# Performance work log

Measured on AMD Instinct MI355X. Metric: run time of the kernel, lower is better.

The kernel has to match this reference:

```python
import jax, jax.numpy as jnp
import numpy as np

EPS = 1e-06

def rmsnorm(x, w):
    x32 = x.astype(jnp.float32)
    var = jnp.mean(x32 * x32, axis=-1, keepdims=True)
    return w * (x32 * jax.lax.rsqrt(var + EPS)).astype(x.dtype)

def setup_inputs() -> dict:
    B, T, C = 16, 256, 16
    token_dim, text_dim = 1024, 512
    key = jax.random.key(0)
    ks = jax.random.split(key, 8)
    token_embeds = jax.random.normal(ks[0], (B, T, token_dim), dtype=jnp.float32)
    char_embeds = jax.random.normal(ks[1], (B, T, C, text_dim), dtype=jnp.float32)
    filler_embed = jax.random.normal(ks[2], (text_dim,), dtype=jnp.float32)
    mask = jax.random.randint(ks[3], (B, T, C), 0, 2).astype(bool)
    mask = mask.at[0].set(True)  # force max valid count == T*C (static output shape)
    token_ids_mask = jnp.ones((B, T), dtype=bool)
    # xavier-uniform-ish weights
    def xav(k, fan_out, fan_in, gain=1.0):
        lim = gain * np.sqrt(6.0 / (fan_in + fan_out))
        return jax.random.uniform(k, (fan_out, fan_in), jnp.float32, -lim, lim)
    W_down = xav(ks[4], text_dim, token_dim)
    W_proj = xav(ks[5], 3, text_dim, gain=0.2)
    W_fusion = xav(ks[6], text_dim, text_dim)
    w_pre = jnp.ones((token_dim,), jnp.float32)
    w_tok = jnp.ones((text_dim,), jnp.float32)
    w_char = jnp.ones((text_dim,), jnp.float32)
    return {"token_embeds": token_embeds, "token_ids_mask": token_ids_mask,
            "char_embeds": char_embeds, "char_ids_mask": mask,
            "filler_embed": filler_embed, "w_pre": w_pre, "w_tok": w_tok,
            "w_char": w_char, "W_down": W_down, "W_proj": W_proj,
            "W_fusion": W_fusion, "max_valid_chars": T * C}

def reference(token_embeds, token_ids_mask, char_embeds, char_ids_mask,
              filler_embed, w_pre, w_tok, w_char, W_down, W_proj, W_fusion,
              max_valid_chars):
    B, T, C, d = char_embeds.shape
    MV = int(max_valid_chars)
    tok = rmsnorm(token_embeds, w_pre)                       # [B,T,token_dim]
    feats = rmsnorm(jnp.einsum('btk,dk->btd', tok, W_down), w_tok)  # [B,T,d]
    params = jnp.einsum('btd,pd->btp', jax.nn.silu(feats), W_proj)  # [B,T,3]
    scale = params[..., 0][:, :, None, None]                 # [B,T,1,1]
    shift = params[..., 1][:, :, None, None]
    gate = jax.nn.sigmoid(params[..., 2][:, :, None, None])
    cn = rmsnorm(char_embeds, w_char)                        # [B,T,C,d]
    fused = jnp.einsum('btcd,ed->btce', jax.nn.silu(cn * (1.0 + scale) + shift), W_fusion)
    fused = gate * fused + (1.0 - gate) * cn                 # [B,T,C,d]
    flat = fused.reshape(B, T * C, d)
    m = char_ids_mask.reshape(B, T * C).astype(jnp.int32)
    pos = jnp.cumsum(m, axis=1) - 1                          # dest within row
    offs = jnp.arange(B, dtype=jnp.int32)[:, None] * MV
    idx = jnp.where(m > 0, offs + pos, B * MV)               # invalid -> dump slot
    buf = jnp.broadcast_to(filler_embed, (B * MV + 1, d))
    buf = buf.at[idx.reshape(-1)].set(flat.reshape(-1, d))
    return buf[: B * MV].reshape(B, MV, d)
```

## Files before the change

### kernel.cpp

```cpp
#include <hip/hip_runtime.h>
#include <cstdint>
#include <cstddef>

#define EPS 1e-6f

typedef short bf16x8 __attribute__((ext_vector_type(8)));
typedef float f32x4  __attribute__((ext_vector_type(4)));

__device__ __forceinline__ short f2bf(float x) {
    uint32_t u = __builtin_bit_cast(uint32_t, x);
    return (short)((u + 0x7FFFu + ((u >> 16) & 1u)) >> 16);
}

__global__ __launch_bounds__(1024) void k_scan(const void* __restrict__ maskp,
                                               int* __restrict__ v_list,
                                               int* __restrict__ counts) {
    __shared__ int wtot[16];
    __shared__ int woff[16];
    __shared__ int mode_s;
    const int tid = threadIdx.x, lane = tid & 63, wave = tid >> 6;
    const int b = blockIdx.x;

    if (tid == 0) mode_s = 0;
    __syncthreads();
    {
        const int bad = (((const uint32_t*)maskp)[tid & 1023] > 1u) ? 1 : 0;
        if (bad) mode_s = 1;
    }
    __syncthreads();
    const int byte_mode = mode_s;

    int f0, f1, f2, f3;
    if (byte_mode) {
        const uint32_t v = ((const uint32_t*)maskp)[(b << 10) + tid];
        f0 = (v & 0x000000ffu) != 0;
        f1 = (v & 0x0000ff00u) != 0;
        f2 = (v & 0x00ff0000u) != 0;
        f3 = (v & 0xff000000u) != 0;
    } else {
        const uint4 v = ((const uint4*)maskp)[(b << 10) + tid];
        f0 = v.x != 0; f1 = v.y != 0; f2 = v.z != 0; f3 = v.w != 0;
    }
    const int c = f0 + f1 + f2 + f3;

    int incl = c;
#pragma unroll
    for (int off = 1; off < 64; off <<= 1) {
        const int n = __shfl_up(incl, off);
        if (lane >= off) incl += n;
    }
    if (lane == 63) wtot[wave] = incl;
    __syncthreads();
    if (tid == 0) {
        int run = 0;
#pragma unroll
        for (int wv = 0; wv < 16; ++wv) { woff[wv] = run; run += wtot[wv]; }
        counts[b] = run;
    }
    __syncthreads();

    int base = woff[wave] + incl - c;
    const int i0 = tid * 4;
    int* vl = v_list + (b << 12);
    if (f0) vl[base++] = i0;
    if (f1) vl[base++] = i0 + 1;
    if (f2) vl[base++] = i0 + 2;
    if (f3) vl[base++] = i0 + 3;
}

__global__ __launch_bounds__(256) void k_conv2(const float* __restrict__ srcA,
                                               short* __restrict__ dstA, int n4a,
                                               const float* __restrict__ srcB,
                                               short* __restrict__ dstB, int n4b) {
    const int gid = blockIdx.x * 256 + threadIdx.x;
    const float* s;
    short* d;
    int i;
    if (gid < n4a) { s = srcA; d = dstA; i = gid; }
    else {
        i = gid - n4a;
        if (i >= n4b) return;
        s = srcB; d = dstB;
    }
    const float4 v = ((const float4*)s)[i];
    short4 o;
    o.x = f2bf(v.x); o.y = f2bf(v.y); o.z = f2bf(v.z); o.w = f2bf(v.w);
    ((short4*)d)[i] = o;
}

__global__ __launch_bounds__(256) void k_tokprep(const float* __restrict__ tokens,
                                                 const float* __restrict__ w_pre,
                                                 short* __restrict__ tokbf) {
    const int tid = threadIdx.x, lane = tid & 63, wave = tid >> 6;
    const int row = blockIdx.x * 4 + wave;
    const float* xp = tokens + (size_t)row * 1024 + lane * 16;
    float4 x[4];
#pragma unroll
    for (int q = 0; q < 4; ++q) x[q] = *(const float4*)&xp[q * 4];
    float ss = 0.f;
#pragma unroll
    for (int q = 0; q < 4; ++q)
        ss += x[q].x * x[q].x + x[q].y * x[q].y + x[q].z * x[q].z + x[q].w * x[q].w;
#pragma unroll
    for (int off = 32; off > 0; off >>= 1) ss += __shfl_down(ss, off);
    ss = __shfl(ss, 0);
    const float r = rsqrtf(ss * (1.0f / 1024.0f) + EPS);
    const float* wp = w_pre + lane * 16;
    short* op = tokbf + (size_t)row * 1024 + lane * 16;
#pragma unroll
    for (int h = 0; h < 2; ++h) {
        bf16x8 o;
#pragma unroll
        for (int q = 0; q < 2; ++q) {
            const float4 wv = *(const float4*)&wp[h * 8 + q * 4];
            const float4 xv = x[h * 2 + q];
            o[q * 4 + 0] = f2bf(xv.x * wv.x * r);
            o[q * 4 + 1] = f2bf(xv.y * wv.y * r);
            o[q * 4 + 2] = f2bf(xv.z * wv.z * r);
            o[q * 4 + 3] = f2bf(xv.w * wv.w * r);
        }
        *(bf16x8*)&op[h * 8] = o;
    }
}

__global__ __launch_bounds__(256) void k_gemm_tok(const short* __restrict__ tokbf,
                                                  const short* __restrict__ Wdbf,
                                                  float* __restrict__ feats) {
    __shared__ short As[128 * 32];
    __shared__ short Bs[128 * 32];
    const int tid = threadIdx.x, lane = tid & 63, w = tid >> 6;
    const int kt = blockIdx.x >> 7;
    const int mt = (blockIdx.x >> 2) & 31, nt = blockIdx.x & 3;
    const int wm = w >> 1, wn = w & 1;
    const int kbase = kt * 512;
    const short* hA = tokbf + (size_t)mt * 128 * 1024;
    const short* wB = Wdbf + (size_t)nt * 128 * 1024;

    f32x4 acc[4][4];
#pragma unroll
    for (int mi = 0; mi < 4; ++mi)
#pragma unroll
        for (int ni = 0; ni < 4; ++ni) acc[mi][ni] = (f32x4)0.f;

    const int rA = lane & 15, q8 = (lane >> 4) * 8;
    for (int kk = 0; kk < 512; kk += 32) {
#pragma unroll
        for (int q = 0; q < 2; ++q) {
            const int cid = (w * 2 + q) * 64 + lane;
            const int r = cid >> 2, kc = cid & 3;
            const size_t go = (size_t)r * 1024 + kbase + kk + kc * 8;
            __builtin_amdgcn_global_load_lds(
                (const __attribute__((address_space(1))) uint32_t*)(hA + go),
                (__attribute__((address_space(3))) uint32_t*)&As[(w * 2 + q) * 512], 16, 0, 0);
            __builtin_amdgcn_global_load_lds(
                (const __attribute__((address_space(1))) uint32_t*)(wB + go),
                (__attribute__((address_space(3))) uint32_t*)&Bs[(w * 2 + q) * 512], 16, 0, 0);
        }
        __syncthreads();
        bf16x8 af[4], bfr[4];
#pragma unroll
        for (int mi = 0; mi < 4; ++mi)
            af[mi] = *(const bf16x8*)&As[(wm * 64 + mi * 16 + rA) * 32 + q8];
#pragma unroll
        for (int ni = 0; ni < 4; ++ni)
            bfr[ni] = *(const bf16x8*)&Bs[(wn * 64 + ni * 16 + rA) * 32 + q8];
#pragma unroll
        for (int mi = 0; mi < 4; ++mi)
#pragma unroll
            for (int ni = 0; ni < 4; ++ni)
                acc[mi][ni] = __builtin_amdgcn_mfma_f32_16x16x32_bf16(af[mi], bfr[ni], acc[mi][ni], 0, 0, 0);
        __syncthreads();
    }
    float* fo = feats + (size_t)kt * 4096 * 512;
    const int rowb = mt * 128 + wm * 64 + (lane >> 4) * 4;
    const int colb = nt * 128 + wn * 64 + (lane & 15);
#pragma unroll
    for (int mi = 0; mi < 4; ++mi)
#pragma unroll
        for (int ni = 0; ni < 4; ++ni)
#pragma unroll
            for (int rg = 0; rg < 4; ++rg)
                fo[(size_t)(rowb + mi * 16 + rg) * 512 + colb + ni * 16] = acc[mi][ni][rg];
}

__global__ __launch_bounds__(64) void k_params(
    const float* __restrict__ feats_pre, const float* __restrict__ w_tok,
    const float* __restrict__ W_proj, float* __restrict__ params) {
    const int tk = blockIdx.x;
    const int lane = threadIdx.x;
    const int d0 = lane * 8;
    const float* fp0 = feats_pre + (size_t)tk * 512 + d0;
    const float* fp1 = fp0 + (size_t)4096 * 512;
    const float4 a0 = *(const float4*)&fp0[0];
    const float4 a1 = *(const float4*)&fp0[4];
    const float4 b0 = *(const float4*)&fp1[0];
    const float4 b1 = *(const float4*)&fp1[4];
    const float4 f0 = make_float4(a0.x + b0.x, a0.y + b0.y, a0.z + b0.z, a0.w + b0.w);
    const float4 f1 = make_float4(a1.x + b1.x, a1.y + b1.y, a1.z + b1.z, a1.w + b1.w);
    float ss = f0.x * f0.x + f0.y * f0.y + f0.z * f0.z + f0.w * f0.w
             + f1.x * f1.x + f1.y * f1.y + f1.z * f1.z + f1.w * f1.w;
#pragma unroll
    for (int off = 32; off > 0; off >>= 1) ss += __shfl_down(ss, off);
    ss = __shfl(ss, 0);
    const float rms = rsqrtf(ss * (1.0f / 512.0f) + EPS);

    const float4 wt0 = *(const float4*)&w_tok[d0];
    const float4 wt1 = *(const float4*)&w_tok[d0 + 4];
    float fv[8] = {f0.x, f0.y, f0.z, f0.w, f1.x, f1.y, f1.z, f1.w};
    float wv[8] = {wt0.x, wt0.y, wt0.z, wt0.w, wt1.x, wt1.y, wt1.z, wt1.w};
    float s[8];
#pragma unroll
    for (int j = 0; j < 8; ++j) {
        const float v = fv[j] * wv[j] * rms;
        s[j] = v / (1.0f + expf(-v));
    }
    float p[3];
#pragma unroll
    for (int q = 0; q < 3; ++q) {
        const float* Wp = W_proj + (size_t)q * 512 + d0;
        const float4 a = *(const float4*)&Wp[0];
        const float4 c = *(const float4*)&Wp[4];
        p[q] = s[0] * a.x + s[1] * a.y + s[2] * a.z + s[3] * a.w
             + s[4] * c.x + s[5] * c.y + s[6] * c.z + s[7] * c.w;
#pragma unroll
        for (int off = 32; off > 0; off >>= 1) p[q] += __shfl_down(p[q], off);
    }
    if (lane == 0) {
        float* po = params + (size_t)tk * 4;
        po[0] = 1.0f + p[0];
        po[1] = p[1];
        po[2] = 1.0f / (1.0f + expf(-p[2]));
    }
}

__global__ __launch_bounds__(256) void k_prep(
    const float* __restrict__ chars, const float* __restrict__ w_char,
    const float* __restrict__ params, const int* __restrict__ v_list,
    const int* __restrict__ counts, short* __restrict__ hb,
    float* __restrict__ rms_l, float* __restrict__ g_l) {
    const int tid = threadIdx.x, lane = tid & 63, wave = tid >> 6;
    const int b = blockIdx.x >> 10;
    const int j = (blockIdx.x & 1023) * 4 + wave;
    const int cnt = counts[b];
    const int cpad = (cnt + 127) & ~127;
    if (j >= cpad) return;
    short* hrow = hb + ((size_t)(b << 12) + j) * 512 + lane * 8;
    if (j >= cnt) {
        *(bf16x8*)hrow = (bf16x8)0;
        return;
    }
    const int i = v_list[(b << 12) + j];
    const float* xp = chars + ((size_t)(b << 12) + i) * 512 + lane * 8;
    const float4 x0 = *(const float4*)&xp[0];
    const float4 x1 = *(const float4*)&xp[4];
    float ss = x0.x * x0.x + x0.y * x0.y + x0.z * x0.z + x0.w * x0.w
             + x1.x * x1.x + x1.y * x1.y + x1.z * x1.z + x1.w * x1.w;
#pragma unroll
    for (int off = 32; off > 0; off >>= 1) ss += __shfl_down(ss, off);
    ss = __shfl(ss, 0);
    const float rms = rsqrtf(ss * (1.0f / 512.0f) + EPS);
    const float* pp = params + (size_t)((b << 8) + (i >> 4)) * 4;
    const float s1 = pp[0], sh = pp[1], g = pp[2];
    const float4 w0 = *(const float4*)&w_char[lane * 8];
    const float4 w1 = *(const float4*)&w_char[lane * 8 + 4];
    float xv[8] = {x0.x, x0.y, x0.z, x0.w, x1.x, x1.y, x1.z, x1.w};
    float wv[8] = {w0.x, w0.y, w0.z, w0.w, w1.x, w1.y, w1.z, w1.w};
    bf16x8 o;
#pragma unroll
    for (int q = 0; q < 8; ++q) {
        const float cn = wv[q] * xv[q] * rms;
        const float a = cn * s1 + sh;
        o[q] = f2bf(a / (1.0f + expf(-a)));
    }
    *(bf16x8*)hrow = o;
    if (lane == 0) {
        rms_l[(b << 12) + j] = rms;
        g_l[(b << 12) + j] = g;
    }
}

__global__ __launch_bounds__(256) void k_gemm_fus(
    const short* __restrict__ hb, const short* __restrict__ Wbf,
    const float* __restrict__ chars, const float* __restrict__ w_char,
    const float* __restrict__ rms_l, const float* __restrict__ g_l,
    const int* __restrict__ v_list, const int* __restrict__ counts,
    const float* __restrict__ filler, float* __restrict__ out) {
    __shared__ short As[128 * 32];
    __shared__ short Bs[128 * 32];
    __shared__ float g_s[128], rms_s[128];
    __shared__ int idx_s[128];
    const int tid = threadIdx.x, lane = tid & 63, w = tid >> 6;
    const int b = blockIdx.x >> 7;
    const int mt = (blockIdx.x >> 2) & 31;
    const int nt = blockIdx.x & 3;
    const int cnt = counts[b];
    const int row0 = mt * 128;
    if (row0 >= cnt) {
        const int colb = nt * 128;
        const float4 f = ((const float4*)(filler + colb))[tid & 31];
        float* o0 = out + ((size_t)(b << 12) + row0) * 512 + colb + (tid & 31) * 4;
#pragma unroll
        for (int r = (tid >> 5); r < 128; r += 8)
            *(float4*)&o0[(size_t)r * 512] = f;
        return;
    }
    const int wm = w >> 1, wn = w & 1;

    if (tid < 128) {
        const int j = row0 + tid;
        const bool valid = j < cnt;
        idx_s[tid] = valid ? v_list[(b << 12) + j] : 0;
        g_s[tid]   = valid ? g_l[(b << 12) + j] : 0.f;
        rms_s[tid] = valid ? rms_l[(b << 12) + j] : 0.f;
    }

    const short* hA = hb + ((size_t)(b << 12) + row0) * 512;
    const short* wB = Wbf + (size_t)nt * 128 * 512;

    f32x4 acc[4][4];
#pragma unroll
    for (int mi = 0; mi < 4; ++mi)
#pragma unroll
        for (int ni = 0; ni < 4; ++ni) acc[mi][ni] = (f32x4)0.f;

    const int rA = lane & 15, q8 = (lane >> 4) * 8;
    for (int kk = 0; kk < 512; kk += 32) {
#pragma unroll
        for (int q = 0; q < 2; ++q) {
            const int cid = (w * 2 + q) * 64 + lane;
            const int r = cid >> 2, kc = cid & 3;
            const size_t go = (size_t)r * 512 + kk + kc * 8;
            __builtin_amdgcn_global_load_lds(
                (const __attribute__((address_space(1))) uint32_t*)(hA + go),
                (__attribute__((address_space(3))) uint32_t*)&As[(w * 2 + q) * 512], 16, 0, 0);
            __builtin_amdgcn_global_load_lds(
                (const __attribute__((address_space(1))) uint32_t*)(wB + go),
                (__attribute__((address_space(3))) uint32_t*)&Bs[(w * 2 + q) * 512], 16, 0, 0);
        }
        __syncthreads();
        bf16x8 af[4], bfr[4];
#pragma unroll
        for (int mi = 0; mi < 4; ++mi)
            af[mi] = *(const bf16x8*)&As[(wm * 64 + mi * 16 + rA) * 32 + q8];
#pragma unroll
        for (int ni = 0; ni < 4; ++ni)
            bfr[ni] = *(const bf16x8*)&Bs[(wn * 64 + ni * 16 + rA) * 32 + q8];
#pragma unroll
        for (int mi = 0; mi < 4; ++mi)
#pragma unroll
            for (int ni = 0; ni < 4; ++ni)
                acc[mi][ni] = __builtin_amdgcn_mfma_f32_16x16x32_bf16(af[mi], bfr[ni], acc[mi][ni], 0, 0, 0);
        __syncthreads();
    }

    const int colb = nt * 128 + wn * 64 + (lane & 15);
    float wcv[4];
#pragma unroll
    for (int ni = 0; ni < 4; ++ni) wcv[ni] = w_char[colb + ni * 16];
#pragma unroll
    for (int mi = 0; mi < 4; ++mi) {
#pragma unroll
        for (int rg = 0; rg < 4; ++rg) {
            const int jl = wm * 64 + mi * 16 + (lane >> 4) * 4 + rg;
            const int j = row0 + jl;
            const size_t orow = ((size_t)(b << 12) + j) * 512;
            if (j < cnt) {
                const float g = g_s[jl], rm = rms_s[jl];
                const size_t xrow = ((size_t)(b << 12) + idx_s[jl]) * 512;
#pragma unroll
                for (int ni = 0; ni < 4; ++ni) {
                    const int col = colb + ni * 16;
                    const float x = chars[xrow + col];
                    const float cn = wcv[ni] * x * rm;
                    out[orow + col] = g * acc[mi][ni][rg] + (1.0f - g) * cn;
                }
            } else {
#pragma unroll
                for (int ni = 0; ni < 4; ++ni) {
                    const int col = colb + ni * 16;
                    out[orow + col] = filler[col];
                }
            }
        }
    }
}

extern "C" void kernel_launch(void* const* d_in, const int* in_sizes, int n_in,
                              void* d_out, int out_size, void* d_ws, size_t ws_size,
                              hipStream_t stream) {
    const float* tokens = (const float*)d_in[0];
    const float* chars  = (const float*)d_in[2];
    const void*  cmask  = d_in[3];
    const float* filler = (const float*)d_in[4];
    const float* w_pre  = (const float*)d_in[5];
    const float* w_tok  = (const float*)d_in[6];
    const float* w_char = (const float*)d_in[7];
    const float* W_down = (const float*)d_in[8];
    const float* W_proj = (const float*)d_in[9];
    const float* W_fus  = (const float*)d_in[10];
    float* out = (float*)d_out;

    float* feats_pre = (float*)d_ws;
    float* params    = feats_pre + (size_t)2 * 4096 * 512;
    int*   counts    = (int*)(params + (size_t)4096 * 4);
    int*   v_list    = counts + 16;
    float* rms_l     = (float*)(v_list + 65536);
    float* g_l       = rms_l + 65536;
    short* Wbf       = (short*)(g_l + 65536);
    short* hb        = Wbf + (size_t)512 * 512;
    short* tokbf     = hb + (size_t)16 * 4096 * 512;
    short* Wdbf      = tokbf + (size_t)4096 * 1024;

    k_scan<<<16, 1024, 0, stream>>>(cmask, v_list, counts);
    k_conv2<<<768, 256, 0, stream>>>(W_fus, Wbf, 65536, W_down, Wdbf, 131072);
    k_tokprep<<<1024, 256, 0, stream>>>(tokens, w_pre, tokbf);
    k_gemm_tok<<<256, 256, 0, stream>>>(tokbf, Wdbf, feats_pre);
    k_params<<<4096, 64, 0, stream>>>(feats_pre, w_tok, W_proj, params);
    k_prep<<<16384, 256, 0, stream>>>(chars, w_char, params, v_list, counts, hb, rms_l, g_l);
    k_gemm_fus<<<2048, 256, 0, stream>>>(hb, Wbf, chars, w_char, rms_l, g_l, v_list, counts, filler, out);
}
```

Before: 339.8 us.

## Fuse char prep into fusion GEMM and merge front kernels into one launch

Removes the separate k_prep kernel. The fusion GEMM now gathers char rows directly, computes the RMS per row, applies the scale/shift SiLU and converts to bf16 on the fly into swizzled LDS, which avoids writing and re-reading the bf16 activation buffer. The scan, weight conversion and token-prep kernels are merged into one launch, and the output stores become nontemporal with a remapped block order. The trade is that each of the four N-tiles per row block recomputes the RMS and the SiLU, and global_load_lds async copies are replaced by register-staged loads.

```diff
diff --git a/kernel.cpp b/kernel.cpp
--- a/kernel.cpp
+++ b/kernel.cpp
@@ -12,114 +12,111 @@
     return (short)((u + 0x7FFFu + ((u >> 16) & 1u)) >> 16);
 }
 
-__global__ __launch_bounds__(1024) void k_scan(const void* __restrict__ maskp,
-                                               int* __restrict__ v_list,
-                                               int* __restrict__ counts) {
-    __shared__ int wtot[16];
-    __shared__ int woff[16];
-    __shared__ int mode_s;
-    const int tid = threadIdx.x, lane = tid & 63, wave = tid >> 6;
-    const int b = blockIdx.x;
-
-    if (tid == 0) mode_s = 0;
-    __syncthreads();
-    {
-        const int bad = (((const uint32_t*)maskp)[tid & 1023] > 1u) ? 1 : 0;
-        if (bad) mode_s = 1;
-    }
-    __syncthreads();
-    const int byte_mode = mode_s;
-
-    int f0, f1, f2, f3;
-    if (byte_mode) {
-        const uint32_t v = ((const uint32_t*)maskp)[(b << 10) + tid];
-        f0 = (v & 0x000000ffu) != 0;
-        f1 = (v & 0x0000ff00u) != 0;
-        f2 = (v & 0x00ff0000u) != 0;
-        f3 = (v & 0xff000000u) != 0;
+__global__ __launch_bounds__(256) void k_front(
+    const void* __restrict__ maskp, int* __restrict__ v_list, int* __restrict__ counts,
+    const float* __restrict__ Wf, short* __restrict__ Wfbf,
+    const float* __restrict__ Wd, short* __restrict__ Wdbf,
+    const float* __restrict__ tokens, const float* __restrict__ w_pre,
+    short* __restrict__ tokbf) {
+    const int blk = blockIdx.x, tid = threadIdx.x;
+    if (blk < 16) {
+        __shared__ int wtot[4], woff[4];
+        __shared__ int mode_s;
+        const int b = blk, lane = tid & 63, wave = tid >> 6;
+        if (tid == 0) mode_s = 0;
+        __syncthreads();
+        {
+            int bad = 0;
+#pragma unroll
+            for (int q = 0; q < 4; ++q)
+                bad |= (((const uint32_t*)maskp)[q * 256 + tid] > 1u) ? 1 : 0;
+            if (bad) mode_s = 1;
+        }
+        __syncthreads();
+        int f[16];
+        if (mode_s) {
+            const uint4 v = ((const uint4*)maskp)[(b << 8) + tid];
+            const uint32_t ws[4] = {v.x, v.y, v.z, v.w};
+#pragma unroll
+            for (int q = 0; q < 4; ++q) {
+                f[q * 4 + 0] = (ws[q] & 0x000000ffu) != 0;
+                f[q * 4 + 1] = (ws[q] & 0x0000ff00u) != 0;
+                f[q * 4 + 2] = (ws[q] & 0x00ff0000u) != 0;
+                f[q * 4 + 3] = (ws[q] & 0xff000000u) != 0;
+            }
+        } else {
+            const uint4* mp = (const uint4*)maskp + ((size_t)b << 10) + tid * 4;
+#pragma unroll
+            for (int q = 0; q < 4; ++q) {
+                const uint4 v = mp[q];
+                f[q * 4 + 0] = v.x != 0; f[q * 4 + 1] = v.y != 0;
+                f[q * 4 + 2] = v.z != 0; f[q * 4 + 3] = v.w != 0;
+            }
+        }
+        int c = 0;
+#pragma unroll
+        for (int q = 0; q < 16; ++q) c += f[q];
+        int incl = c;
+#pragma unroll
+        for (int off = 1; off < 64; off <<= 1) {
+            const int n = __shfl_up(incl, off);
+            if (lane >= off) incl += n;
+        }
+        if (lane == 63) wtot[wave] = incl;
+        __syncthreads();
+        if (tid == 0) {
+            int run = 0;
+#pragma unroll
+            for (int wv = 0; wv < 4; ++wv) { woff[wv] = run; run += wtot[wv]; }
+            counts[b] = run;
+        }
+        __syncthreads();
+        int base = woff[wave] + incl - c;
+        int* vl = v_list + (b << 12);
+        const int i0 = tid * 16;
+#pragma unroll
+        for (int q = 0; q < 16; ++q)
+            if (f[q]) vl[base++] = i0 + q;
+    } else if (blk < 784) {
+        const int gid = (blk - 16) * 256 + tid;
+        const float* s; short* d; int i;
+        if (gid < 65536) { s = Wf; d = Wfbf; i = gid; }
+        else             { s = Wd; d = Wdbf; i = gid - 65536; }
+        const float4 v = ((const float4*)s)[i];
+        short4 o;
+        o.x = f2bf(v.x); o.y = f2bf(v.y); o.z = f2bf(v.z); o.w = f2bf(v.w);
+        ((short4*)d)[i] = o;
     } else {
-        const uint4 v = ((const uint4*)maskp)[(b << 10) + tid];
-        f0 = v.x != 0; f1 = v.y != 0; f2 = v.z != 0; f3 = v.w != 0;
-    }
-    const int c = f0 + f1 + f2 + f3;
-
-    int incl = c;
-#pragma unroll
-    for (int off = 1; off < 64; off <<= 1) {
-        const int n = __shfl_up(incl, off);
-        if (lane >= off) incl += n;
-    }
-    if (lane == 63) wtot[wave] = incl;
-    __syncthreads();
-    if (tid == 0) {
-        int run = 0;
-#pragma unroll
-        for (int wv = 0; wv < 16; ++wv) { woff[wv] = run; run += wtot[wv]; }
-        counts[b] = run;
-    }
-    __syncthreads();
-
-    int base = woff[wave] + incl - c;
-    const int i0 = tid * 4;
-    int* vl = v_list + (b << 12);
-    if (f0) vl[base++] = i0;
-    if (f1) vl[base++] = i0 + 1;
-    if (f2) vl[base++] = i0 + 2;
-    if (f3) vl[base++] = i0 + 3;
-}
-
-__global__ __launch_bounds__(256) void k_conv2(const float* __restrict__ srcA,
-                                               short* __restrict__ dstA, int n4a,
-                                               const float* __restrict__ srcB,
-                                               short* __restrict__ dstB, int n4b) {
-    const int gid = blockIdx.x * 256 + threadIdx.x;
-    const float* s;
-    short* d;
-    int i;
-    if (gid < n4a) { s = srcA; d = dstA; i = gid; }
-    else {
-        i = gid - n4a;
-        if (i >= n4b) return;
-        s = srcB; d = dstB;
-    }
-    const float4 v = ((const float4*)s)[i];
-    short4 o;
-    o.x = f2bf(v.x); o.y = f2bf(v.y); o.z = f2bf(v.z); o.w = f2bf(v.w);
-    ((short4*)d)[i] = o;
-}
-
-__global__ __launch_bounds__(256) void k_tokprep(const float* __restrict__ tokens,
-                                                 const float* __restrict__ w_pre,
-                                                 short* __restrict__ tokbf) {
-    const int tid = threadIdx.x, lane = tid & 63, wave = tid >> 6;
-    const int row = blockIdx.x * 4 + wave;
-    const float* xp = tokens + (size_t)row * 1024 + lane * 16;
-    float4 x[4];
-#pragma unroll
-    for (int q = 0; q < 4; ++q) x[q] = *(const float4*)&xp[q * 4];
-    float ss = 0.f;
-#pragma unroll
-    for (int q = 0; q < 4; ++q)
-        ss += x[q].x * x[q].x + x[q].y * x[q].y + x[q].z * x[q].z + x[q].w * x[q].w;
-#pragma unroll
-    for (int off = 32; off > 0; off >>= 1) ss += __shfl_down(ss, off);
-    ss = __shfl(ss, 0);
-    const float r = rsqrtf(ss * (1.0f / 1024.0f) + EPS);
-    const float* wp = w_pre + lane * 16;
-    short* op = tokbf + (size_t)row * 1024 + lane * 16;
-#pragma unroll
-    for (int h = 0; h < 2; ++h) {
-        bf16x8 o;
-#pragma unroll
-        for (int q = 0; q < 2; ++q) {
-            const float4 wv = *(const float4*)&wp[h * 8 + q * 4];
-            const float4 xv = x[h * 2 + q];
-            o[q * 4 + 0] = f2bf(xv.x * wv.x * r);
-            o[q * 4 + 1] = f2bf(xv.y * wv.y * r);
-            o[q * 4 + 2] = f2bf(xv.z * wv.z * r);
-            o[q * 4 + 3] = f2bf(xv.w * wv.w * r);
-        }
-        *(bf16x8*)&op[h * 8] = o;
+        const int lane = tid & 63, wave = tid >> 6;
+        const int row = (blk - 784) * 4 + wave;
+        const float* xp = tokens + (size_t)row * 1024 + lane * 16;
+        float4 x[4];
+#pragma unroll
+        for (int q = 0; q < 4; ++q) x[q] = *(const float4*)&xp[q * 4];
+        float ss = 0.f;
+#pragma unroll
+        for (int q = 0; q < 4; ++q)
+            ss += x[q].x * x[q].x + x[q].y * x[q].y + x[q].z * x[q].z + x[q].w * x[q].w;
+#pragma unroll
+        for (int off = 32; off > 0; off >>= 1) ss += __shfl_down(ss, off);
+        ss = __shfl(ss, 0);
+        const float r = rsqrtf(ss * (1.0f / 1024.0f) + EPS);
+        const float* wp = w_pre + lane * 16;
+        short* op = tokbf + (size_t)row * 1024 + lane * 16;
+#pragma unroll
+        for (int h = 0; h < 2; ++h) {
+            bf16x8 o;
+#pragma unroll
+            for (int q = 0; q < 2; ++q) {
+                const float4 wv = *(const float4*)&wp[h * 8 + q * 4];
+                const float4 xv = x[h * 2 + q];
+                o[q * 4 + 0] = f2bf(xv.x * wv.x * r);
+                o[q * 4 + 1] = f2bf(xv.y * wv.y * r);
+                o[q * 4 + 2] = f2bf(xv.z * wv.z * r);
+                o[q * 4 + 3] = f2bf(xv.w * wv.w * r);
+            }
+            *(bf16x8*)&op[h * 8] = o;
+        }
     }
 }
 
@@ -230,121 +227,136 @@
         po[0] = 1.0f + p[0];
         po[1] = p[1];
         po[2] = 1.0f / (1.0f + expf(-p[2]));
-    }
-}
-
-__global__ __launch_bounds__(256) void k_prep(
-    const float* __restrict__ chars, const float* __restrict__ w_char,
-    const float* __restrict__ params, const int* __restrict__ v_list,
-    const int* __restrict__ counts, short* __restrict__ hb,
-    float* __restrict__ rms_l, float* __restrict__ g_l) {
-    const int tid = threadIdx.x, lane = tid & 63, wave = tid >> 6;
-    const int b = blockIdx.x >> 10;
-    const int j = (blockIdx.x & 1023) * 4 + wave;
-    const int cnt = counts[b];
-    const int cpad = (cnt + 127) & ~127;
-    if (j >= cpad) return;
-    short* hrow = hb + ((size_t)(b << 12) + j) * 512 + lane * 8;
-    if (j >= cnt) {
-        *(bf16x8*)hrow = (bf16x8)0;
-        return;
-    }
-    const int i = v_list[(b << 12) + j];
-    const float* xp = chars + ((size_t)(b << 12) + i) * 512 + lane * 8;
-    const float4 x0 = *(const float4*)&xp[0];
-    const float4 x1 = *(const float4*)&xp[4];
-    float ss = x0.x * x0.x + x0.y * x0.y + x0.z * x0.z + x0.w * x0.w
-             + x1.x * x1.x + x1.y * x1.y + x1.z * x1.z + x1.w * x1.w;
-#pragma unroll
-    for (int off = 32; off > 0; off >>= 1) ss += __shfl_down(ss, off);
-    ss = __shfl(ss, 0);
-    const float rms = rsqrtf(ss * (1.0f / 512.0f) + EPS);
-    const float* pp = params + (size_t)((b << 8) + (i >> 4)) * 4;
-    const float s1 = pp[0], sh = pp[1], g = pp[2];
-    const float4 w0 = *(const float4*)&w_char[lane * 8];
-    const float4 w1 = *(const float4*)&w_char[lane * 8 + 4];
-    float xv[8] = {x0.x, x0.y, x0.z, x0.w, x1.x, x1.y, x1.z, x1.w};
-    float wv[8] = {w0.x, w0.y, w0.z, w0.w, w1.x, w1.y, w1.z, w1.w};
-    bf16x8 o;
-#pragma unroll
-    for (int q = 0; q < 8; ++q) {
-        const float cn = wv[q] * xv[q] * rms;
-        const float a = cn * s1 + sh;
-        o[q] = f2bf(a / (1.0f + expf(-a)));
-    }
-    *(bf16x8*)hrow = o;
-    if (lane == 0) {
-        rms_l[(b << 12) + j] = rms;
-        g_l[(b << 12) + j] = g;
+        po[3] = 0.f;
     }
 }
 
 __global__ __launch_bounds__(256) void k_gemm_fus(
-    const short* __restrict__ hb, const short* __restrict__ Wbf,
-    const float* __restrict__ chars, const float* __restrict__ w_char,
-    const float* __restrict__ rms_l, const float* __restrict__ g_l,
+    const short* __restrict__ Wbf, const float* __restrict__ chars,
+    const float* __restrict__ w_char, const float* __restrict__ params,
     const int* __restrict__ v_list, const int* __restrict__ counts,
     const float* __restrict__ filler, float* __restrict__ out) {
-    __shared__ short As[128 * 32];
-    __shared__ short Bs[128 * 32];
-    __shared__ float g_s[128], rms_s[128];
-    __shared__ int idx_s[128];
+    const int wg = (blockIdx.x & 7) * 256 + (blockIdx.x >> 3);
+    const int b = wg >> 7;
+    const int mt = (wg >> 2) & 31;
+    const int nt = wg & 3;
     const int tid = threadIdx.x, lane = tid & 63, w = tid >> 6;
-    const int b = blockIdx.x >> 7;
-    const int mt = (blockIdx.x >> 2) & 31;
-    const int nt = blockIdx.x & 3;
     const int cnt = counts[b];
     const int row0 = mt * 128;
     if (row0 >= cnt) {
-        const int colb = nt * 128;
-        const float4 f = ((const float4*)(filler + colb))[tid & 31];
-        float* o0 = out + ((size_t)(b << 12) + row0) * 512 + colb + (tid & 31) * 4;
-#pragma unroll
-        for (int r = (tid >> 5); r < 128; r += 8)
-            *(float4*)&o0[(size_t)r * 512] = f;
+        const int colb0 = nt * 128;
+        const f32x4 f = *(const f32x4*)(filler + colb0 + (tid & 31) * 4);
+        float* o0 = out + ((size_t)(b << 12) + row0) * 512 + colb0 + (tid & 31) * 4;
+        for (int r = tid >> 5; r < 128; r += 8)
+            __builtin_nontemporal_store(f, (f32x4*)&o0[(size_t)r * 512]);
         return;
     }
-    const int wm = w >> 1, wn = w & 1;
+
+    __shared__ short As[128 * 32];
+    __shared__ short Bs[128 * 32];
+    __shared__ float wc_s[512];
+    __shared__ float rmsv[128], s1v[128], shv[128], gv[128];
+    __shared__ int idxv[128];
+
+    wc_s[tid] = w_char[tid];
+    wc_s[tid + 256] = w_char[tid + 256];
 
     if (tid < 128) {
         const int j = row0 + tid;
         const bool valid = j < cnt;
-        idx_s[tid] = valid ? v_list[(b << 12) + j] : 0;
-        g_s[tid]   = valid ? g_l[(b << 12) + j] : 0.f;
-        rms_s[tid] = valid ? rms_l[(b << 12) + j] : 0.f;
-    }
-
-    const short* hA = hb + ((size_t)(b << 12) + row0) * 512;
-    const short* wB = Wbf + (size_t)nt * 128 * 512;
-
+        const int idx = valid ? v_list[(b << 12) + j] : -1;
+        idxv[tid] = idx;
+        if (valid) {
+            const float* pp = params + (size_t)((b << 8) + (idx >> 4)) * 4;
+            s1v[tid] = pp[0]; shv[tid] = pp[1]; gv[tid] = pp[2];
+        } else {
+            s1v[tid] = 0.f; shv[tid] = 0.f; gv[tid] = 0.f;
+        }
+    }
+    __syncthreads();
+
+    {
+        const int g16 = tid >> 4, l16 = tid & 15;
+#pragma unroll
+        for (int rr = 0; rr < 8; ++rr) {
+            const int r = g16 * 8 + rr;
+            const int id = idxv[r];
+            float ss = 0.f;
+            if (id >= 0) {
+                const float* rp = chars + (((size_t)(b << 12) + id) << 9) + l16 * 4;
+#pragma unroll
+                for (int s = 0; s < 8; ++s) {
+                    const float4 v = *(const float4*)&rp[s * 64];
+                    ss += v.x * v.x + v.y * v.y + v.z * v.z + v.w * v.w;
+                }
+            }
+#pragma unroll
+            for (int off = 8; off > 0; off >>= 1) ss += __shfl_down(ss, off);
+            if (l16 == 0) rmsv[r] = rsqrtf(ss * (1.0f / 512.0f) + EPS);
+        }
+    }
+    __syncthreads();
+
+    const int wm = w >> 1, wn = w & 1;
     f32x4 acc[4][4];
 #pragma unroll
     for (int mi = 0; mi < 4; ++mi)
 #pragma unroll
         for (int ni = 0; ni < 4; ++ni) acc[mi][ni] = (f32x4)0.f;
 
-    const int rA = lane & 15, q8 = (lane >> 4) * 8;
+    const int r2 = tid >> 1, hf = tid & 1;
+    const int swzA = ((r2 >> 1) & 3) << 3;
+    const float rmsr = rmsv[r2], s1r = s1v[r2], shr = shv[r2];
+    const int idr = idxv[r2];
+    const float* arow = (idr >= 0) ? (chars + (((size_t)(b << 12) + idr) << 9)) : nullptr;
+    const short* brow = Wbf + ((size_t)(nt * 128 + r2) << 9) + hf * 16;
+
+    const int rA = lane & 15;
+    const int ch = lane >> 4;
+
     for (int kk = 0; kk < 512; kk += 32) {
-#pragma unroll
-        for (int q = 0; q < 2; ++q) {
-            const int cid = (w * 2 + q) * 64 + lane;
-            const int r = cid >> 2, kc = cid & 3;
-            const size_t go = (size_t)r * 512 + kk + kc * 8;
-            __builtin_amdgcn_global_load_lds(
-                (const __attribute__((address_space(1))) uint32_t*)(hA + go),
-                (__attribute__((address_space(3))) uint32_t*)&As[(w * 2 + q) * 512], 16, 0, 0);
-            __builtin_amdgcn_global_load_lds(
-                (const __attribute__((address_space(1))) uint32_t*)(wB + go),
-                (__attribute__((address_space(3))) uint32_t*)&Bs[(w * 2 + q) * 512], 16, 0, 0);
-        }
-        __syncthreads();
+        const bf16x8 b0 = *(const bf16x8*)&brow[kk];
+        const bf16x8 b1 = *(const bf16x8*)&brow[kk + 8];
+        bf16x8 a0, a1;
+        if (idr >= 0) {
+            const float* ap = arow + kk + hf * 16;
+            const float4 x0 = *(const float4*)&ap[0];
+            const float4 x1 = *(const float4*)&ap[4];
+            const float4 x2 = *(const float4*)&ap[8];
+            const float4 x3 = *(const float4*)&ap[12];
+            const float xv[16] = {x0.x, x0.y, x0.z, x0.w, x1.x, x1.y, x1.z, x1.w,
+                                  x2.x, x2.y, x2.z, x2.w, x3.x, x3.y, x3.z, x3.w};
+            const float* wcp = &wc_s[kk + hf * 16];
+            short tmp[16];
+#pragma unroll
+            for (int q = 0; q < 16; ++q) {
+                const float cn = wcp[q] * xv[q] * rmsr;
+                const float a = cn * s1r + shr;
+                tmp[q] = f2bf(a / (1.0f + expf(-a)));
+            }
+#pragma unroll
+            for (int q = 0; q < 8; ++q) { a0[q] = tmp[q]; a1[q] = tmp[q + 8]; }
+        } else {
+            a0 = (bf16x8)0; a1 = (bf16x8)0;
+        }
+        const int base = r2 * 32;
+        *(bf16x8*)&As[base + (((hf * 2 + 0) << 3) ^ swzA)] = a0;
+        *(bf16x8*)&As[base + (((hf * 2 + 1) << 3) ^ swzA)] = a1;
+        *(bf16x8*)&Bs[base + (((hf * 2 + 0) << 3) ^ swzA)] = b0;
+        *(bf16x8*)&Bs[base + (((hf * 2 + 1) << 3) ^ swzA)] = b1;
+        __syncthreads();
+
         bf16x8 af[4], bfr[4];
 #pragma unroll
-        for (int mi = 0; mi < 4; ++mi)
-            af[mi] = *(const bf16x8*)&As[(wm * 64 + mi * 16 + rA) * 32 + q8];
-#pragma unroll
-        for (int ni = 0; ni < 4; ++ni)
-            bfr[ni] = *(const bf16x8*)&Bs[(wn * 64 + ni * 16 + rA) * 32 + q8];
+        for (int mi = 0; mi < 4; ++mi) {
+            const int row = wm * 64 + mi * 16 + rA;
+            af[mi] = *(const bf16x8*)&As[row * 32 + ((ch ^ ((row >> 1) & 3)) << 3)];
+        }
+#pragma unroll
+        for (int ni = 0; ni < 4; ++ni) {
+            const int row = wn * 64 + ni * 16 + rA;
+            bfr[ni] = *(const bf16x8*)&Bs[row * 32 + ((ch ^ ((row >> 1) & 3)) << 3)];
+        }
 #pragma unroll
         for (int mi = 0; mi < 4; ++mi)
 #pragma unroll
@@ -356,7 +368,7 @@
     const int colb = nt * 128 + wn * 64 + (lane & 15);
     float wcv[4];
 #pragma unroll
-    for (int ni = 0; ni < 4; ++ni) wcv[ni] = w_char[colb + ni * 16];
+    for (int ni = 0; ni < 4; ++ni) wcv[ni] = wc_s[colb + ni * 16];
 #pragma unroll
     for (int mi = 0; mi < 4; ++mi) {
 #pragma unroll
@@ -365,20 +377,21 @@
             const int j = row0 + jl;
             const size_t orow = ((size_t)(b << 12) + j) * 512;
             if (j < cnt) {
-                const float g = g_s[jl], rm = rms_s[jl];
-                const size_t xrow = ((size_t)(b << 12) + idx_s[jl]) * 512;
+                const float g = gv[jl], rm = rmsv[jl];
+                const size_t xrow = ((size_t)(b << 12) + idxv[jl]) * 512;
 #pragma unroll
                 for (int ni = 0; ni < 4; ++ni) {
                     const int col = colb + ni * 16;
                     const float x = chars[xrow + col];
                     const float cn = wcv[ni] * x * rm;
-                    out[orow + col] = g * acc[mi][ni][rg] + (1.0f - g) * cn;
+                    __builtin_nontemporal_store(g * acc[mi][ni][rg] + (1.0f - g) * cn,
+                                                &out[orow + col]);
                 }
             } else {
 #pragma unroll
                 for (int ni = 0; ni < 4; ++ni) {
                     const int col = colb + ni * 16;
-                    out[orow + col] = filler[col];
+                    __builtin_nontemporal_store(filler[col], &out[orow + col]);
                 }
             }
         }
@@ -404,18 +417,14 @@
     float* params    = feats_pre + (size_t)2 * 4096 * 512;
     int*   counts    = (int*)(params + (size_t)4096 * 4);
     int*   v_list    = counts + 16;
-    float* rms_l     = (float*)(v_list + 65536);
-    float* g_l       = rms_l + 65536;
-    short* Wbf       = (short*)(g_l + 65536);
-    short* hb        = Wbf + (size_t)512 * 512;
-    short* tokbf     = hb + (size_t)16 * 4096 * 512;
+    short* Wbf       = (short*)(v_list + 65536);
+    short* tokbf     = Wbf + (size_t)512 * 512;
     short* Wdbf      = tokbf + (size_t)4096 * 1024;
 
-    k_scan<<<16, 1024, 0, stream>>>(cmask, v_list, counts);
-    k_conv2<<<768, 256, 0, stream>>>(W_fus, Wbf, 65536, W_down, Wdbf, 131072);
-    k_tokprep<<<1024, 256, 0, stream>>>(tokens, w_pre, tokbf);
+    k_front<<<1808, 256, 0, stream>>>(cmask, v_list, counts, W_fus, Wbf,
+                                      W_down, Wdbf, tokens, w_pre, tokbf);
     k_gemm_tok<<<256, 256, 0, stream>>>(tokbf, Wdbf, feats_pre);
     k_params<<<4096, 64, 0, stream>>>(feats_pre, w_tok, W_proj, params);
-    k_prep<<<16384, 256, 0, stream>>>(chars, w_char, params, v_list, counts, hb, rms_l, g_l);
-    k_gemm_fus<<<2048, 256, 0, stream>>>(hb, Wbf, chars, w_char, rms_l, g_l, v_list, counts, filler, out);
-}
+    k_gemm_fus<<<2048, 256, 0, stream>>>(Wbf, chars, w_char, params,
+                                         v_list, counts, filler, out);
+}
```

After: 419.7 us. 1.24x slower.
